# Optimization experiments

Hardware: AMD Instinct MI355X
Metric: run time of the kernel (lower is better)

Reference implementation:

```python
import math
import jax, jax.numpy as jnp
import numpy as np

S = 2048   # padded sequence length (both src and tgt)
B = 8      # batch
D = 512    # d_embed
K = 64     # num_neighbors


def setup_inputs() -> dict:
    key = jax.random.key(0)
    ks = jax.random.split(key, 12)
    f32 = jnp.float32
    src_feats = jax.random.normal(ks[0], (S, B, D), f32)
    tgt_feats = jax.random.normal(ks[1], (S, B, D), f32)
    src_xyz = jax.random.normal(ks[2], (S, B, 3), f32)
    tgt_xyz = jax.random.normal(ks[3], (S, B, 3), f32)
    # lengths in [S - S//8, S] so every row has plenty of valid keys (>= K)
    src_lens = S - jax.random.randint(ks[4], (B,), 0, S // 8)
    tgt_lens = S - jax.random.randint(ks[5], (B,), 0, S // 8)
    scale = 1.0 / math.sqrt(D)
    Wq = jax.random.normal(ks[6], (D, D), f32) * scale
    bq = jnp.zeros((D,), f32)
    Wk = jax.random.normal(ks[7], (D, D), f32) * scale
    bk = jnp.zeros((D,), f32)
    Wc = jax.random.normal(ks[8], (1, D), f32) * scale
    bc = jnp.zeros((1,), f32)
    return dict(src_feats_padded=src_feats, tgt_feats_padded=tgt_feats,
                src_xyz_padded=src_xyz, tgt_xyz_padded=tgt_xyz,
                src_lens=src_lens, tgt_lens=tgt_lens,
                Wq=Wq, bq=bq, Wk=Wk, bk=bk, Wc=Wc, bc=bc)


def _simple_attention(query, key, value, key_padding_mask, Wq, bq, Wk, bk, num_neighbors):
    # query: (Q,B,D), key: (S,B,D), value: (S,B,E), key_padding_mask: (B,S) True=pad
    d = query.shape[-1]
    q = (query @ Wq.T + bq) / math.sqrt(d)          # (Q,B,D)
    k = key @ Wk.T + bk                              # (S,B,D)
    attn = jnp.einsum('qbd,sbd->bqs', q, k)          # (B,Q,S)
    attn = attn + jnp.where(key_padding_mask, -jnp.inf, 0.0)[:, None, :]
    if num_neighbors > 0:
        # Faithful to torch's `neighbor_mask[:, :, haha] = 0` (advanced indexing):
        # the UNION of top-k column indices over all (b,q) rows is unmasked for
        # every row; all other columns get -inf.
        idx = jax.lax.top_k(attn, num_neighbors)[1]              # (B,Q,K)
        col_mask = jnp.full((attn.shape[-1],), -jnp.inf, attn.dtype)
        col_mask = col_mask.at[idx.reshape(-1)].set(0.0)         # (S,)
        attn = attn + col_mask[None, None, :]
    attn = jax.nn.softmax(attn, axis=-1)
    return jnp.einsum('bqs,sbe->qbe', attn, value)   # (Q,B,E)


def _forward(src_feats, tgt_feats, src_xyz, tgt_xyz, src_lens, tgt_lens,
             Wq, bq, Wk, bk, Wc, bc):
    n_src, b = src_feats.shape[0], src_feats.shape[1]
    n_tgt = tgt_feats.shape[0]
    src_kpm = jnp.arange(n_src)[None, :] >= src_lens[:, None]   # (B,N_src)
    tgt_kpm = jnp.arange(n_tgt)[None, :] >= tgt_lens[:, None]   # (B,N_tgt)
    src_corr = _simple_attention(src_feats, tgt_feats, tgt_xyz, tgt_kpm,
                                 Wq, bq, Wk, bk, K)             # (N_src,B,3)
    tgt_corr = _simple_attention(tgt_feats, src_feats, src_xyz, src_kpm,
                                 Wq, bq, Wk, bk, K)             # (N_tgt,B,3)
    src_overlap = src_feats @ Wc.T + bc                          # (N_src,B,1)
    tgt_overlap = tgt_feats @ Wc.T + bc                          # (N_tgt,B,1)
    return src_corr, tgt_corr, src_overlap, tgt_overlap


def reference(src_feats_padded, tgt_feats_padded, src_xyz_padded, tgt_xyz_padded,
              src_lens, tgt_lens, Wq, bq, Wk, bk, Wc, bc):
    return _forward(src_feats_padded, tgt_feats_padded, src_xyz_padded,
                    tgt_xyz_padded, src_lens, tgt_lens, Wq, bq, Wk, bk, Wc, bc)
```

## Files before the change

### kernel.cpp

```cpp
#include <hip/hip_runtime.h>

typedef __attribute__((ext_vector_type(8))) short short8;
typedef __attribute__((ext_vector_type(4))) float f32x4;

#define SEQ 2048
#define BAT 8
#define DIM 512
#define RSQRT_D 0.044194173824159216f

__device__ __forceinline__ unsigned short f2bf(float x) {
  union { float f; unsigned u; } v; v.f = x;
  unsigned r = (v.u + 0x7FFFu + ((v.u >> 16) & 1u)) >> 16;
  return (unsigned short)r;
}

__device__ __forceinline__ unsigned char f2fp8(float x) {
  return (unsigned char)(__builtin_amdgcn_cvt_pk_fp8_f32(x, x, 0, false) & 0xFF);
}

__device__ __forceinline__ void gload_lds16(const void* g, void* lds_base) {
  __builtin_amdgcn_global_load_lds(
      (const __attribute__((address_space(1))) unsigned int*)g,
      (__attribute__((address_space(3))) unsigned int*)lds_base,
      16, 0, 0);
}

__global__ __launch_bounds__(256) void k_pack(
    const float* __restrict__ src, const float* __restrict__ tgt,
    const float* __restrict__ Wc, const float* __restrict__ bc,
    const float* __restrict__ sxyz, const float* __restrict__ txyz,
    const float* __restrict__ Wq, const float* __restrict__ Wk,
    unsigned short* __restrict__ srcT, unsigned short* __restrict__ tgtT,
    float4* __restrict__ Vsrc, float4* __restrict__ Vtgt,
    unsigned short* __restrict__ Wqb, unsigned short* __restrict__ Wkb,
    float* __restrict__ out) {
  int which = blockIdx.y;
  if (blockIdx.x >= 4096) {
    int e = (blockIdx.x - 4096) * 256 + threadIdx.x;
    if (which == 0) {
      int wsel = e >> 15, j = e & 32767;
      const float* wp = (wsel ? Wk : Wq) + (size_t)j * 8;
      unsigned short* o = wsel ? Wkb : Wqb;
      float4 f0 = *(const float4*)wp, f1 = *(const float4*)(wp + 4);
      uint4 pk;
      pk.x = (unsigned)f2bf(f0.x) | ((unsigned)f2bf(f0.y) << 16);
      pk.y = (unsigned)f2bf(f0.z) | ((unsigned)f2bf(f0.w) << 16);
      pk.z = (unsigned)f2bf(f1.x) | ((unsigned)f2bf(f1.y) << 16);
      pk.w = (unsigned)f2bf(f1.z) | ((unsigned)f2bf(f1.w) << 16);
      *(uint4*)(o + (size_t)j * 8) = pk;
    } else if (e < 32768) {
      int wsel = e >> 14, id = e & 16383;
      int s = id >> 3, b = id & 7;
      const float* xyz = (wsel ? txyz : sxyz) + (size_t)id * 3;
      float4 v = make_float4(xyz[0], xyz[1], xyz[2], 0.f);
      (wsel ? Vtgt : Vsrc)[b * SEQ + s] = v;
    }
    return;
  }
  int w = threadIdx.x >> 6, lane = threadIdx.x & 63;
  int row = blockIdx.x * 4 + w;
  const float* in = (which ? tgt : src) + (size_t)row * DIM;
  unsigned short* T = which ? tgtT : srcT;
  int s = row >> 3, b = row & 7;

  const float4* in4 = (const float4*)in;
  float4 f0 = in4[lane * 2], f1 = in4[lane * 2 + 1];

  uint4 pk;
  pk.x = (unsigned)f2bf(f0.x) | ((unsigned)f2bf(f0.y) << 16);
  pk.y = (unsigned)f2bf(f0.z) | ((unsigned)f2bf(f0.w) << 16);
  pk.z = (unsigned)f2bf(f1.x) | ((unsigned)f2bf(f1.y) << 16);
  pk.w = (unsigned)f2bf(f1.z) | ((unsigned)f2bf(f1.w) << 16);
  *(uint4*)(T + ((size_t)(b * SEQ + s) * DIM + lane * 8)) = pk;

  const float4* wc4 = (const float4*)Wc;
  float4 w0 = wc4[lane * 2], w1 = wc4[lane * 2 + 1];
  float d = f0.x * w0.x + f0.y * w0.y + f0.z * w0.z + f0.w * w0.w +
            f1.x * w1.x + f1.y * w1.y + f1.z * w1.z + f1.w * w1.w;
  for (int o = 32; o; o >>= 1) d += __shfl_xor(d, o);
  if (lane == 0) {
    int base = which ? (SEQ * BAT * 6 + SEQ * BAT) : (SEQ * BAT * 6);
    out[base + row] = d + bc[0];
  }
}

__global__ __launch_bounds__(256) void k_proj(
    const unsigned short* __restrict__ srcT, const unsigned short* __restrict__ tgtT,
    const unsigned short* __restrict__ Wqb, const unsigned short* __restrict__ Wkb,
    const float* __restrict__ bq, const float* __restrict__ bk,
    unsigned char* __restrict__ Qsrc, unsigned char* __restrict__ Ktgt,
    unsigned char* __restrict__ Qtgt, unsigned char* __restrict__ Ksrc) {
  __shared__ __align__(16) char at[16384];
  __shared__ __align__(16) char bt[16384];
  int id = blockIdx.x;
  int x = id & 7, t = id >> 3;
  int m = x * 16 + (t >> 4);
  int inner = t & 15;
  int n = inner & 3, z = inner >> 2;
  bool isQ = (z == 0 || z == 2);
  const unsigned short* A = (z == 0 || z == 3) ? srcT : tgtT;
  const unsigned short* W = isQ ? Wqb : Wkb;
  const float* bias = isQ ? bq : bk;
  unsigned char* O = z == 0 ? Qsrc : z == 1 ? Ktgt : z == 2 ? Qtgt : Ksrc;

  int m0 = m * 128, n0 = n * 128;
  int tid = threadIdx.x, w = tid >> 6, lane = tid & 63;
  int ln = lane & 15, quad = lane >> 4;
  int moff = (w & 1) * 64, noff = (w >> 1) * 64;

  f32x4 acc[4][4];
  f32x4 zero = {0.f, 0.f, 0.f, 0.f};
  for (int mi = 0; mi < 4; ++mi)
    for (int ni = 0; ni < 4; ++ni) acc[mi][ni] = zero;

  for (int kb = 0; kb < DIM; kb += 64) {
    #pragma unroll
    for (int it = 0; it < 4; ++it) {
      int rbase = w * 32 + it * 8;
      int r = rbase + (lane >> 3);
      int c = (lane & 7) ^ (r & 7);
      gload_lds16(A + ((size_t)(m0 + r) * DIM + kb + c * 8), &at[rbase * 128]);
      gload_lds16(W + ((size_t)(n0 + r) * DIM + kb + c * 8), &bt[rbase * 128]);
    }
    __syncthreads();
    #pragma unroll
    for (int ks = 0; ks < 2; ++ks) {
      short8 afr[4], bfr[4];
      #pragma unroll
      for (int mi = 0; mi < 4; ++mi) {
        int r = moff + mi * 16 + ln;
        int p = (ks * 4 + quad) ^ (r & 7);
        afr[mi] = *(const short8*)(&at[r * 128 + p * 16]);
      }
      #pragma unroll
      for (int ni = 0; ni < 4; ++ni) {
        int r = noff + ni * 16 + ln;
        int p = (ks * 4 + quad) ^ (r & 7);
        bfr[ni] = *(const short8*)(&bt[r * 128 + p * 16]);
      }
      #pragma unroll
      for (int mi = 0; mi < 4; ++mi)
        #pragma unroll
        for (int ni = 0; ni < 4; ++ni)
          acc[mi][ni] = __builtin_amdgcn_mfma_f32_16x16x32_bf16(afr[mi], bfr[ni], acc[mi][ni], 0, 0, 0);
    }
    __syncthreads();
  }

  for (int ni = 0; ni < 4; ++ni) {
    int n_g = n0 + noff + ni * 16 + ln;
    float bv = bias[n_g];
    for (int mi = 0; mi < 4; ++mi) {
      int m_g = m0 + moff + mi * 16 + quad * 4;
      for (int r = 0; r < 4; ++r) {
        float v = acc[mi][ni][r] + bv;
        int row = m_g + r;
        size_t pos;
        if (isQ) pos = (size_t)row * DIM + n_g;
        else     pos = (size_t)row * DIM + ((((n_g >> 3) ^ (row & 15)) << 3) | (n_g & 7));
        O[pos] = f2fp8(v);
      }
    }
  }
}

__global__ __launch_bounds__(256) void k_attn(
    const unsigned char* __restrict__ Qsrc, const unsigned char* __restrict__ Ktgt,
    const unsigned char* __restrict__ Qtgt, const unsigned char* __restrict__ Ksrc,
    const float4* __restrict__ Vsrc, const float4* __restrict__ Vtgt,
    const int* __restrict__ src_lens, const int* __restrict__ tgt_lens,
    float4* __restrict__ part) {
  __shared__ __align__(16) char klds[16384];
  __shared__ float vx[512], vy[512], vz[512];
  int id = blockIdx.x;
  int x = id & 7, j = id >> 3;
  int group = (j >> 7) * 8 + x;
  int dir = group >> 3, b = group & 7;
  int inner = j & 127;
  int chunk = inner >> 5, qb = inner & 31;

  const unsigned char* Q = dir ? Qtgt : Qsrc;
  const unsigned char* K = dir ? Ksrc : Ktgt;
  const float4* V = dir ? Vsrc : Vtgt;
  int len = (dir ? src_lens : tgt_lens)[b];
  int k0g = chunk * 512;
  int kend = min(len, k0g + 512);
  int nblk = (kend - k0g + 31) >> 5;

  int tid = threadIdx.x, w = tid >> 6, lane = tid & 63;
  int ln = lane & 15, quad = lane >> 4;
  int q0 = qb * 64 + w * 16;

  for (int i = tid; i < 512; i += 256) {
    float4 vv = V[b * SEQ + k0g + i];
    vx[i] = vv.x; vy[i] = vv.y; vz[i] = vv.z;
  }

  long af[16];
  {
    const unsigned char* qrow = Q + (size_t)(b * SEQ + q0 + ln) * DIM + quad * 8;
    #pragma unroll
    for (int kk = 0; kk < 16; ++kk)
      af[kk] = *(const long*)(qrow + kk * 32);
  }

  float l_r[4], Ox[4], Oy[4], Oz[4];
  #pragma unroll
  for (int r = 0; r < 4; ++r) { l_r[r] = 0.f; Ox[r] = Oy[r] = Oz[r] = 0.f; }

  const unsigned char* kchunk = K + (size_t)(b * SEQ + k0g) * DIM;

  for (int kb = 0; kb < nblk; ++kb) {
    const unsigned char* kbase = kchunk + (size_t)kb * 32 * DIM;
    #pragma unroll
    for (int it = 0; it < 4; ++it) {
      int rp = w * 4 + it;
      gload_lds16(kbase + rp * 1024 + lane * 16, &klds[rp * 1024]);
    }
    __syncthreads();

    const char* krow0 = klds + ln * DIM;
    const char* krow1 = klds + (16 + ln) * DIM;

    f32x4 acc0 = {0.f, 0.f, 0.f, 0.f}, acc1 = {0.f, 0.f, 0.f, 0.f};
    #pragma unroll
    for (int kk = 0; kk < 16; ++kk) {
      int pos = (((kk * 4 + quad) ^ ln) << 3);
      long b0 = *(const long*)(krow0 + pos);
      long b1 = *(const long*)(krow1 + pos);
      acc0 = __builtin_amdgcn_mfma_f32_16x16x32_fp8_fp8(af[kk], b0, acc0, 0, 0, 0);
      acc1 = __builtin_amdgcn_mfma_f32_16x16x32_fp8_fp8(af[kk], b1, acc1, 0, 0, 0);
    }

    int lk0 = kb * 32 + ln, lk1 = lk0 + 16;
    bool v0 = (k0g + lk0) < kend, v1 = (k0g + lk1) < kend;
    float Vx0 = vx[lk0], Vy0 = vy[lk0], Vz0 = vz[lk0];
    float Vx1 = vx[lk1], Vy1 = vy[lk1], Vz1 = vz[lk1];
    #pragma unroll
    for (int r = 0; r < 4; ++r) {
      float p0 = v0 ? __expf(acc0[r] * RSQRT_D) : 0.f;
      float p1 = v1 ? __expf(acc1[r] * RSQRT_D) : 0.f;
      l_r[r] += p0 + p1;
      Ox[r] += p0 * Vx0 + p1 * Vx1;
      Oy[r] += p0 * Vy0 + p1 * Vy1;
      Oz[r] += p0 * Vz0 + p1 * Vz1;
    }
    __syncthreads();
  }

  #pragma unroll
  for (int r = 0; r < 4; ++r) {
    float v0 = l_r[r], v1 = Ox[r], v2 = Oy[r], v3 = Oz[r];
    #pragma unroll
    for (int o = 1; o < 16; o <<= 1) {
      v0 += __shfl_xor(v0, o);
      v1 += __shfl_xor(v1, o);
      v2 += __shfl_xor(v2, o);
      v3 += __shfl_xor(v3, o);
    }
    if (ln == 0) {
      int q = q0 + quad * 4 + r;
      part[((size_t)(dir * BAT + b) * 4 + chunk) * SEQ + q] =
          make_float4(v0, v1, v2, v3);
    }
  }
}

__global__ __launch_bounds__(256) void k_attn_reduce(
    const float4* __restrict__ part, float* __restrict__ out) {
  int t = blockIdx.x * 256 + threadIdx.x;
  int dir = t >> 14, rem = t & 16383, b = rem >> 11, q = rem & 2047;
  size_t base = ((size_t)(dir * BAT + b) * 4) * SEQ + q;
  float4 s0 = part[base];
  float4 s1 = part[base + SEQ];
  float4 s2 = part[base + 2 * SEQ];
  float4 s3 = part[base + 3 * SEQ];
  float inv = 1.f / (s0.x + s1.x + s2.x + s3.x);
  float* ob = out + (size_t)dir * (SEQ * BAT * 3) + ((size_t)q * BAT + b) * 3;
  ob[0] = (s0.y + s1.y + s2.y + s3.y) * inv;
  ob[1] = (s0.z + s1.z + s2.z + s3.z) * inv;
  ob[2] = (s0.w + s1.w + s2.w + s3.w) * inv;
}

extern "C" void kernel_launch(void* const* d_in, const int* in_sizes, int n_in,
                              void* d_out, int out_size, void* d_ws, size_t ws_size,
                              hipStream_t stream) {
  const float* src  = (const float*)d_in[0];
  const float* tgt  = (const float*)d_in[1];
  const float* sxyz = (const float*)d_in[2];
  const float* txyz = (const float*)d_in[3];
  const int* slens  = (const int*)d_in[4];
  const int* tlens  = (const int*)d_in[5];
  const float* Wq   = (const float*)d_in[6];
  const float* bq   = (const float*)d_in[7];
  const float* Wk   = (const float*)d_in[8];
  const float* bk   = (const float*)d_in[9];
  const float* Wc   = (const float*)d_in[10];
  const float* bc   = (const float*)d_in[11];
  float* out = (float*)d_out;

  char* ws = (char*)d_ws;
  size_t off = 0;
  auto carve = [&](size_t bytes) -> char* {
    char* p = ws + off;
    off += (bytes + 255) & ~(size_t)255;
    return p;
  };
  const size_t FEAT_BF  = (size_t)BAT * SEQ * DIM * 2;
  const size_t FEAT_FP8 = (size_t)BAT * SEQ * DIM;
  unsigned short* srcT = (unsigned short*)carve(FEAT_BF);
  unsigned short* tgtT = (unsigned short*)carve(FEAT_BF);
  unsigned char* Qsrc = (unsigned char*)carve(FEAT_FP8);
  unsigned char* Ktgt = (unsigned char*)carve(FEAT_FP8);
  unsigned char* Qtgt = (unsigned char*)carve(FEAT_FP8);
  unsigned char* Ksrc = (unsigned char*)carve(FEAT_FP8);
  unsigned short* Wqb  = (unsigned short*)carve((size_t)DIM * DIM * 2);
  unsigned short* Wkb  = (unsigned short*)carve((size_t)DIM * DIM * 2);
  float4* Vsrc = (float4*)carve((size_t)BAT * SEQ * 16);
  float4* Vtgt = (float4*)carve((size_t)BAT * SEQ * 16);
  float4* part = (float4*)srcT;

  k_pack<<<dim3(4352, 2), 256, 0, stream>>>(src, tgt, Wc, bc, sxyz, txyz, Wq, Wk,
                                            srcT, tgtT, Vsrc, Vtgt, Wqb, Wkb, out);
  k_proj<<<dim3(2048), 256, 0, stream>>>(srcT, tgtT, Wqb, Wkb, bq, bk,
                                         Qsrc, Ktgt, Qtgt, Ksrc);
  k_attn<<<dim3(2048), 256, 0, stream>>>(Qsrc, Ktgt, Qtgt, Ksrc, Vsrc, Vtgt,
                                         slens, tlens, part);
  k_attn_reduce<<<dim3(128), 256, 0, stream>>>(part, out);
}
```

Measured before the change: 247.0 us.

## Compute P·V with bf16 MFMA against an augmented [1,x,y,z] value tile

Replaces the scalar per-row softmax-weighted accumulation of the row sum and xyz with a bf16 16x16x16 MFMA. It multiplies exp scores, packed to bf16, by an LDS tile holding a ones column plus x, y, z. The QK MFMA operands are swapped so the score layout matches the PV MFMA input, and the validity mask moves into the augmented V, whose invalid rows are zeroed. This drops the cross-lane shuffle reduction at the end and adds s_setprio around the QK MFMAs. The trade-off is bf16 rounding of probabilities and V coordinates, which may cost accuracy.

```diff
diff --git a/kernel.cpp b/kernel.cpp
--- a/kernel.cpp
+++ b/kernel.cpp
@@ -1,6 +1,7 @@
 #include <hip/hip_runtime.h>
 
 typedef __attribute__((ext_vector_type(8))) short short8;
+typedef __attribute__((ext_vector_type(4))) short s16x4;
 typedef __attribute__((ext_vector_type(4))) float f32x4;
 
 #define SEQ 2048
@@ -23,6 +24,11 @@
       (const __attribute__((address_space(1))) unsigned int*)g,
       (__attribute__((address_space(3))) unsigned int*)lds_base,
       16, 0, 0);
+}
+
+__device__ __forceinline__ f32x4 mfma_pv(s16x4 a, s16x4 b, f32x4 c) {
+  asm("v_mfma_f32_16x16x16_bf16 %0, %1, %2, %0" : "+v"(c) : "v"(a), "v"(b));
+  return c;
 }
 
 __global__ __launch_bounds__(256) void k_pack(
@@ -171,7 +177,7 @@
     const int* __restrict__ src_lens, const int* __restrict__ tgt_lens,
     float4* __restrict__ part) {
   __shared__ __align__(16) char klds[16384];
-  __shared__ float vx[512], vy[512], vz[512];
+  __shared__ __align__(16) char vaug[4096];
   int id = blockIdx.x;
   int x = id & 7, j = id >> 3;
   int group = (j >> 7) * 8 + x;
@@ -191,9 +197,30 @@
   int ln = lane & 15, quad = lane >> 4;
   int q0 = qb * 64 + w * 16;
 
-  for (int i = tid; i < 512; i += 256) {
-    float4 vv = V[b * SEQ + k0g + i];
-    vx[i] = vv.x; vy[i] = vv.y; vz[i] = vv.z;
+  if (tid < 128) {
+    int rem = kend - k0g;
+    const float4* vsrc = V + b * SEQ + k0g + tid * 4;
+    float c[4][4];
+    #pragma unroll
+    for (int jj = 0; jj < 4; ++jj) {
+      float4 vv = vsrc[jj];
+      bool val = (tid * 4 + jj) < rem;
+      c[0][jj] = val ? 1.f : 0.f;
+      c[1][jj] = val ? vv.x : 0.f;
+      c[2][jj] = val ? vv.y : 0.f;
+      c[3][jj] = val ? vv.z : 0.f;
+    }
+    uint4 w0, w1;
+    w0.x = (unsigned)f2bf(c[0][0]) | ((unsigned)f2bf(c[0][1]) << 16);
+    w0.y = (unsigned)f2bf(c[0][2]) | ((unsigned)f2bf(c[0][3]) << 16);
+    w0.z = (unsigned)f2bf(c[1][0]) | ((unsigned)f2bf(c[1][1]) << 16);
+    w0.w = (unsigned)f2bf(c[1][2]) | ((unsigned)f2bf(c[1][3]) << 16);
+    w1.x = (unsigned)f2bf(c[2][0]) | ((unsigned)f2bf(c[2][1]) << 16);
+    w1.y = (unsigned)f2bf(c[2][2]) | ((unsigned)f2bf(c[2][3]) << 16);
+    w1.z = (unsigned)f2bf(c[3][0]) | ((unsigned)f2bf(c[3][1]) << 16);
+    w1.w = (unsigned)f2bf(c[3][2]) | ((unsigned)f2bf(c[3][3]) << 16);
+    *(uint4*)(vaug + tid * 32) = w0;
+    *(uint4*)(vaug + tid * 32 + 16) = w1;
   }
 
   long af[16];
@@ -204,10 +231,7 @@
       af[kk] = *(const long*)(qrow + kk * 32);
   }
 
-  float l_r[4], Ox[4], Oy[4], Oz[4];
-  #pragma unroll
-  for (int r = 0; r < 4; ++r) { l_r[r] = 0.f; Ox[r] = Oy[r] = Oz[r] = 0.f; }
-
+  f32x4 accPV = {0.f, 0.f, 0.f, 0.f};
   const unsigned char* kchunk = K + (size_t)(b * SEQ + k0g) * DIM;
 
   for (int kb = 0; kb < nblk; ++kb) {
@@ -220,49 +244,48 @@
     __syncthreads();
 
     const char* krow0 = klds + ln * DIM;
-    const char* krow1 = klds + (16 + ln) * DIM;
+    const char* krow1 = krow0 + 16 * DIM;
 
     f32x4 acc0 = {0.f, 0.f, 0.f, 0.f}, acc1 = {0.f, 0.f, 0.f, 0.f};
+    __builtin_amdgcn_s_setprio(1);
     #pragma unroll
     for (int kk = 0; kk < 16; ++kk) {
       int pos = (((kk * 4 + quad) ^ ln) << 3);
       long b0 = *(const long*)(krow0 + pos);
       long b1 = *(const long*)(krow1 + pos);
-      acc0 = __builtin_amdgcn_mfma_f32_16x16x32_fp8_fp8(af[kk], b0, acc0, 0, 0, 0);
-      acc1 = __builtin_amdgcn_mfma_f32_16x16x32_fp8_fp8(af[kk], b1, acc1, 0, 0, 0);
-    }
-
-    int lk0 = kb * 32 + ln, lk1 = lk0 + 16;
-    bool v0 = (k0g + lk0) < kend, v1 = (k0g + lk1) < kend;
-    float Vx0 = vx[lk0], Vy0 = vy[lk0], Vz0 = vz[lk0];
-    float Vx1 = vx[lk1], Vy1 = vy[lk1], Vz1 = vz[lk1];
-    #pragma unroll
-    for (int r = 0; r < 4; ++r) {
-      float p0 = v0 ? __expf(acc0[r] * RSQRT_D) : 0.f;
-      float p1 = v1 ? __expf(acc1[r] * RSQRT_D) : 0.f;
-      l_r[r] += p0 + p1;
-      Ox[r] += p0 * Vx0 + p1 * Vx1;
-      Oy[r] += p0 * Vy0 + p1 * Vy1;
-      Oz[r] += p0 * Vz0 + p1 * Vz1;
-    }
+      acc0 = __builtin_amdgcn_mfma_f32_16x16x32_fp8_fp8(b0, af[kk], acc0, 0, 0, 0);
+      acc1 = __builtin_amdgcn_mfma_f32_16x16x32_fp8_fp8(b1, af[kk], acc1, 0, 0, 0);
+    }
+    __builtin_amdgcn_s_setprio(0);
+
+    unsigned u00, u01, u10, u11;
+    {
+      float p0 = __expf(acc0[0] * RSQRT_D), p1 = __expf(acc0[1] * RSQRT_D);
+      float p2 = __expf(acc0[2] * RSQRT_D), p3 = __expf(acc0[3] * RSQRT_D);
+      asm("v_cvt_pk_bf16_f32 %0, %1, %2" : "=v"(u00) : "v"(p0), "v"(p1));
+      asm("v_cvt_pk_bf16_f32 %0, %1, %2" : "=v"(u01) : "v"(p2), "v"(p3));
+      float r0 = __expf(acc1[0] * RSQRT_D), r1 = __expf(acc1[1] * RSQRT_D);
+      float r2 = __expf(acc1[2] * RSQRT_D), r3 = __expf(acc1[3] * RSQRT_D);
+      asm("v_cvt_pk_bf16_f32 %0, %1, %2" : "=v"(u10) : "v"(r0), "v"(r1));
+      asm("v_cvt_pk_bf16_f32 %0, %1, %2" : "=v"(u11) : "v"(r2), "v"(r3));
+    }
+    union U { unsigned u[2]; s16x4 s; };
+    U pb0; pb0.u[0] = u00; pb0.u[1] = u01;
+    U pb1; pb1.u[0] = u10; pb1.u[1] = u11;
+
+    int voff = kb * 256 + quad * 32 + (ln & 3) * 8;
+    s16x4 va0 = *(const s16x4*)(vaug + voff);
+    s16x4 va1 = *(const s16x4*)(vaug + voff + 128);
+    accPV = mfma_pv(va0, pb0.s, accPV);
+    accPV = mfma_pv(va1, pb1.s, accPV);
+
     __syncthreads();
   }
 
-  #pragma unroll
-  for (int r = 0; r < 4; ++r) {
-    float v0 = l_r[r], v1 = Ox[r], v2 = Oy[r], v3 = Oz[r];
-    #pragma unroll
-    for (int o = 1; o < 16; o <<= 1) {
-      v0 += __shfl_xor(v0, o);
-      v1 += __shfl_xor(v1, o);
-      v2 += __shfl_xor(v2, o);
-      v3 += __shfl_xor(v3, o);
-    }
-    if (ln == 0) {
-      int q = q0 + quad * 4 + r;
-      part[((size_t)(dir * BAT + b) * 4 + chunk) * SEQ + q] =
-          make_float4(v0, v1, v2, v3);
-    }
+  if (quad == 0) {
+    int q = q0 + ln;
+    part[((size_t)(dir * BAT + b) * 4 + chunk) * SEQ + q] =
+        make_float4(accPV[0], accPV[1], accPV[2], accPV[3]);
   }
 }
 
```

Result: faster. 238.4 us (-3.5%).
